# Kernel optimization log

Measured on AMD Instinct MI355X. Metric: run time of the kernel, lower is better.

The kernel has to match this reference:

```python
import jax, jax.numpy as jnp
import numpy as np

U = 256    # hp.hidden_size * 2 (attention num_units / encoder dim)
H = 128    # hp.hidden_size (prenet output, attn GRU input)
MEL = 80   # hp.decoder_output_dim == hp.num_mels
R = 5      # hp.outputs_per_step
B = 64
T = 1000


def _glorot(key, shape):
    fan_in = shape[-1]
    return jax.random.normal(key, shape, jnp.float32) / jnp.sqrt(jnp.float32(fan_in))


def setup_inputs() -> dict:
    key = jax.random.key(0)
    ks = jax.random.split(key, 16)
    p = {}
    p["memory"] = jax.random.normal(ks[0], (B, T, U), jnp.float32)
    # prenet: fc1 (MEL->U), fc2 (U->H)
    p["Wp1"] = _glorot(ks[1], (U, MEL)); p["bp1"] = jnp.zeros((U,), jnp.float32)
    p["Wp2"] = _glorot(ks[2], (H, U));   p["bp2"] = jnp.zeros((H,), jnp.float32)
    # Bahdanau attention params (no bias)
    p["W1"] = _glorot(ks[3], (U, U))
    p["W2"] = _glorot(ks[4], (U, U))
    p["v"]  = _glorot(ks[5], (U,))
    def gru(k, din):
        k1, k2 = jax.random.split(k)
        return (_glorot(k1, (3 * U, din)), _glorot(k2, (3 * U, U)),
                jnp.zeros((3 * U,), jnp.float32), jnp.zeros((3 * U,), jnp.float32))
    p["Wa_ih"], p["Wa_hh"], p["ba_ih"], p["ba_hh"] = gru(ks[6], H)
    p["W1_ih"], p["W1_hh"], p["b1_ih"], p["b1_hh"] = gru(ks[7], U)
    p["W2_ih"], p["W2_hh"], p["b2_ih"], p["b2_hh"] = gru(ks[8], U)
    p["Wproj"] = _glorot(ks[9], (U, 2 * U)); p["bproj"] = jnp.zeros((U,), jnp.float32)
    p["Wout"] = _glorot(ks[10], (MEL * R, U)); p["bout"] = jnp.zeros((MEL * R,), jnp.float32)
    return p


def _gru_cell(x, h, W_ih, W_hh, b_ih, b_hh):
    # torch.nn.GRUCell semantics
    gi = x @ W_ih.T + b_ih
    gh = h @ W_hh.T + b_hh
    ir, iz, inn = jnp.split(gi, 3, axis=-1)
    hr, hz, hn = jnp.split(gh, 3, axis=-1)
    r = jax.nn.sigmoid(ir + hr)
    z = jax.nn.sigmoid(iz + hz)
    n = jnp.tanh(inn + r * hn)
    return (1.0 - z) * n + z * h


def reference(memory, Wp1, bp1, Wp2, bp2, W1, W2, v,
              Wa_ih, Wa_hh, ba_ih, ba_hh,
              W1_ih, W1_hh, b1_ih, b1_hh,
              W2_ih, W2_hh, b2_ih, b2_hh,
              Wproj, bproj, Wout, bout):
    b, t, u = memory.shape
    steps = t // R  # training branch: timesteps = memory_len // outputs_per_step
    # keys = W1(memory): constant across timesteps, hoist out of the loop
    keys = jnp.einsum('btu,vu->btv', memory, W1)
    init = (jnp.zeros((b, MEL), memory.dtype),  # prev mel frame (GO frame = zeros)
            jnp.zeros((b, u), memory.dtype),    # attn_hidden
            jnp.zeros((b, u), memory.dtype),    # gru1_hidden
            jnp.zeros((b, u), memory.dtype))    # gru2_hidden

    def step(carry, _):
        prev, attn_h, g1_h, g2_h = carry
        # prenet (dropout omitted for determinism; identity in eval mode)
        x = jax.nn.relu(prev @ Wp1.T + bp1)
        x = jax.nn.relu(x @ Wp2.T + bp2)
        # attention query through GRU cell
        d_t = _gru_cell(x, attn_h, Wa_ih, Wa_hh, ba_ih, ba_hh)
        q = d_t @ W2.T                                     # [b,u]
        scores = jnp.tanh(keys + q[:, None, :]) @ v       # [b,t]
        aw = jax.nn.softmax(scores, axis=1)
        d_t_prime = jnp.einsum('bt,btu->bu', aw, memory)   # context
        # residual GRU stack
        g1_in = jnp.concatenate([d_t, d_t_prime], axis=1) @ Wproj.T + bproj
        g1_h = _gru_cell(g1_in, g1_h, W1_ih, W1_hh, b1_ih, b1_hh)
        g2_in = g1_in + g1_h
        g2_h = _gru_cell(g2_in, g2_h, W2_ih, W2_hh, b2_ih, b2_hh)
        out = ((g2_in + g2_h) @ Wout.T + bout).reshape(b, MEL, R)
        return (out[:, :, -1], d_t, g1_h, g2_h), out

    _, ys = jax.lax.scan(step, init, None, length=steps)   # [steps,b,MEL,R]
    # torch.cat(outputs, 2) -> [b, MEL, steps*R]
    return jnp.transpose(ys, (1, 2, 0, 3)).reshape(b, MEL, steps * R)
```

## Files before the change

### kernel.cpp

```cpp
#include <hip/hip_runtime.h>

typedef _Float16 f16;
typedef _Float16 h2 __attribute__((ext_vector_type(2)));
typedef float fv4 __attribute__((ext_vector_type(4)));

#define BB 64
#define UU 256
#define RRR 5
#define NQUAD 4

constexpr size_t O_WP1T = 0;
constexpr size_t O_WP2T = 10240;
constexpr size_t O_WAIH = 26624;
constexpr size_t O_WAHH = 75776;
constexpr size_t O_WQP  = 174080;
constexpr size_t O_WPC  = 239616;
constexpr size_t O_W1IH = 272384;
constexpr size_t O_W1HH = 370688;
constexpr size_t O_W2IH = 468992;
constexpr size_t O_W2HH = 567296;
constexpr size_t O_WOUT = 665600;
constexpr size_t OF_BQP = 716800;
constexpr size_t OF_W1T = 717312;
constexpr size_t OH_KEYS = 1565696;
constexpr size_t OH_MEM  = OH_KEYS + 16384000;
constexpr size_t OF_CTXP  = 17166848;
constexpr size_t OF_ESUM  = 17297920;
constexpr size_t OF_QB    = 17298432;
constexpr size_t OI_FLAGA = 17331200;
constexpr size_t OI_FLAGB = 17347584;

#define SCL2LOG2E 2.8853900817779268f

#if defined(__has_builtin)
#if __has_builtin(__builtin_amdgcn_fdot2)
#define USE_FDOT2 1
#endif
#endif

__device__ __forceinline__ float dot2f(h2 a, h2 b, float c){
#ifdef USE_FDOT2
  return __builtin_amdgcn_fdot2(a, b, c, false);
#else
  return c + (float)a[0]*(float)b[0] + (float)a[1]*(float)b[1];
#endif
}

__device__ __forceinline__ float frcp(float x){ return __builtin_amdgcn_rcpf(x); }
__device__ __forceinline__ float fexp2(float x){ return __builtin_amdgcn_exp2f(x); }
__device__ __forceinline__ float fsig(float x){ return frcp(1.0f + fexp2(-1.4426950408889634f*x)); }
__device__ __forceinline__ float ftanh(float x){ return 1.0f - 2.0f*frcp(1.0f + fexp2(SCL2LOG2E*x)); }

__device__ __forceinline__ void wait_flag(const int* fl, int target){
  while (__hip_atomic_load(fl, __ATOMIC_RELAXED, __HIP_MEMORY_SCOPE_AGENT) < target){
    __builtin_amdgcn_s_sleep(8);
  }
  (void)__hip_atomic_load(fl, __ATOMIC_ACQUIRE, __HIP_MEMORY_SCOPE_AGENT);
}

__global__ void k_tr_hx(const float* __restrict__ src, int srcK, int kbase,
                        h2* __restrict__ dst, int N, int K, int Ntot, int coloff,
                        float scale){
  int idx = blockIdx.x*blockDim.x + threadIdx.x;
  int tot = N*(K/2);
  if (idx < tot){
    int k2 = idx / N, n = idx - k2*N;
    h2 p; p[0]=(f16)(scale*src[n*srcK + kbase + 2*k2]);
    p[1]=(f16)(scale*src[n*srcK + kbase + 2*k2+1]);
    dst[(size_t)k2*Ntot + coloff + n] = p;
  }
}

__global__ void k_transpose(const float* __restrict__ src, float* __restrict__ dst, int N, int K){
  int idx = blockIdx.x*blockDim.x + threadIdx.x;
  if (idx < N*K){
    int n = idx / K, k = idx - n*K;
    dst[k*N + n] = src[idx];
  }
}

__global__ void k_biasqp(const float* __restrict__ bproj, float* __restrict__ dst){
  int i = blockIdx.x*blockDim.x + threadIdx.x;
  if (i < 512) dst[i] = (i < 256) ? 0.f : bproj[i-256];
}

__global__ void k_zero(int* __restrict__ p, int n){
  int i = blockIdx.x*blockDim.x + threadIdx.x;
  if (i < n) p[i] = 0;
}

__global__ void k_memh(const float* __restrict__ src, f16* __restrict__ dst, int n8){
  int i = blockIdx.x*blockDim.x + threadIdx.x;
  if (i < n8){
    const float4* s = reinterpret_cast<const float4*>(src) + 2*(size_t)i;
    float4 f0 = s[0], f1 = s[1];
    union { f16 h[8]; float4 v; } u;
    u.h[0]=(f16)f0.x; u.h[1]=(f16)f0.y; u.h[2]=(f16)f0.z; u.h[3]=(f16)f0.w;
    u.h[4]=(f16)f1.x; u.h[5]=(f16)f1.y; u.h[6]=(f16)f1.z; u.h[7]=(f16)f1.w;
    reinterpret_cast<float4*>(dst)[i] = u.v;
  }
}

__global__ __launch_bounds__(256) void k_keys(const float* __restrict__ mem,
      const float* __restrict__ W1t, f16* __restrict__ keys, int T)
{
  const int b = blockIdx.z;
  const int tbase = blockIdx.x * 128;
  const int cbase = blockIdx.y * 128;
  const int tid = threadIdx.x;
  const int rt = tid >> 4, ct = tid & 15;
  const float* memb = mem + (size_t)b*T*UU;

  float acc[8][8];
  #pragma unroll
  for (int i=0;i<8;i++){
    #pragma unroll
    for (int j=0;j<8;j++) acc[i][j]=0.f;
  }
  const float* arow[8];
  #pragma unroll
  for (int i=0;i<8;i++){
    int t = tbase + rt*8 + i;
    arow[i] = memb + (size_t)(t < T ? t : T-1)*UU;
  }
  const float* wcol = W1t + cbase + ct*8;

  for (int k=0;k<UU;k+=4){
    float w8[4][8];
    #pragma unroll
    for (int kk=0;kk<4;kk++){
      float4 lo = *reinterpret_cast<const float4*>(wcol + (size_t)(k+kk)*UU);
      float4 hi = *reinterpret_cast<const float4*>(wcol + (size_t)(k+kk)*UU + 4);
      w8[kk][0]=lo.x; w8[kk][1]=lo.y; w8[kk][2]=lo.z; w8[kk][3]=lo.w;
      w8[kk][4]=hi.x; w8[kk][5]=hi.y; w8[kk][6]=hi.z; w8[kk][7]=hi.w;
    }
    #pragma unroll
    for (int i=0;i<8;i++){
      float4 a = *reinterpret_cast<const float4*>(arow[i] + k);
      float a4[4] = {a.x, a.y, a.z, a.w};
      #pragma unroll
      for (int kk=0;kk<4;kk++){
        #pragma unroll
        for (int j=0;j<8;j++) acc[i][j] += a4[kk]*w8[kk][j];
      }
    }
  }
  #pragma unroll
  for (int i=0;i<8;i++){
    int t = tbase + rt*8 + i;
    if (t < T){
      f16* dst = keys + (size_t)b*T*UU + (size_t)t*UU + cbase + ct*8;
      union { f16 h[8]; float4 v; } u;
      #pragma unroll
      for (int j=0;j<8;j++) u.h[j] = (f16)(acc[i][j]*SCL2LOG2E);
      *reinterpret_cast<float4*>(dst) = u.v;
    }
  }
}

__device__ __attribute__((noinline)) void gemv_shfl(
    const h2* __restrict__ W, const h2* __restrict__ in,
    const float* __restrict__ bias, float* __restrict__ destf, h2* __restrict__ desth,
    int K2, int Nf4, int act, int local)
{
  const int lane = local & 63;
  const int half = lane >> 5;
  int col = (local >> 6)*32 + (lane & 31);
  const bool valid = col < Nf4;
  if (!valid) col = 0;
  const int kh = K2 >> 1;
  const float4* w = reinterpret_cast<const float4*>(W) + (size_t)(half*kh)*Nf4 + col;
  const h2* ia = in + half*kh;
  float a0=0.f, a1=0.f, a2=0.f, a3=0.f;
  #pragma unroll 8
  for (int it = 0; it < kh; ++it){
    float4 wp = w[(size_t)it*Nf4];
    h2 a = ia[it];
    const h2* wh = reinterpret_cast<const h2*>(&wp);
    a0 = dot2f(wh[0], a, a0);
    a1 = dot2f(wh[1], a, a1);
    a2 = dot2f(wh[2], a, a2);
    a3 = dot2f(wh[3], a, a3);
  }
  a0 += __shfl_xor(a0, 32, 64);
  a1 += __shfl_xor(a1, 32, 64);
  a2 += __shfl_xor(a2, 32, 64);
  a3 += __shfl_xor(a3, 32, 64);
  if (half == 0 && valid){
    if (bias){
      const float4 bv = reinterpret_cast<const float4*>(bias)[col];
      a0+=bv.x; a1+=bv.y; a2+=bv.z; a3+=bv.w;
    }
    if (act == 1){
      a0=fmaxf(a0,0.f); a1=fmaxf(a1,0.f); a2=fmaxf(a2,0.f); a3=fmaxf(a3,0.f);
    } else if (act == 2){
      const float4 d = reinterpret_cast<float4*>(destf)[col];
      a0+=d.x; a1+=d.y; a2+=d.z; a3+=d.w;
    }
    if (destf){
      float4 r; r.x=a0; r.y=a1; r.z=a2; r.w=a3;
      reinterpret_cast<float4*>(destf)[col] = r;
    }
    if (desth){
      h2 p0; p0[0]=(f16)a0; p0[1]=(f16)a1;
      h2 p1; p1[0]=(f16)a2; p1[1]=(f16)a3;
      desth[2*col] = p0; desth[2*col+1] = p1;
    }
  }
}

__device__ __attribute__((noinline)) void gemv_shfl4(
    const h2* __restrict__ W, const h2* __restrict__ in,
    const float* __restrict__ bias, float* __restrict__ destf, h2* __restrict__ desth,
    int K2, int Nf4, int act, int local)
{
  const int lane = local & 63;
  const int qtr  = lane >> 4;
  int col = (local >> 6)*16 + (lane & 15);
  const bool valid = col < Nf4;
  if (!valid) col = 0;
  const int kq = K2 >> 2;
  const float4* w = reinterpret_cast<const float4*>(W) + (size_t)(qtr*kq)*Nf4 + col;
  const h2* ia = in + qtr*kq;
  float a0=0.f, a1=0.f, a2=0.f, a3=0.f;
  #pragma unroll 8
  for (int it = 0; it < kq; ++it){
    float4 wp = w[(size_t)it*Nf4];
    h2 a = ia[it];
    const h2* wh = reinterpret_cast<const h2*>(&wp);
    a0 = dot2f(wh[0], a, a0);
    a1 = dot2f(wh[1], a, a1);
    a2 = dot2f(wh[2], a, a2);
    a3 = dot2f(wh[3], a, a3);
  }
  a0 += __shfl_xor(a0, 16, 64); a1 += __shfl_xor(a1, 16, 64);
  a2 += __shfl_xor(a2, 16, 64); a3 += __shfl_xor(a3, 16, 64);
  a0 += __shfl_xor(a0, 32, 64); a1 += __shfl_xor(a1, 32, 64);
  a2 += __shfl_xor(a2, 32, 64); a3 += __shfl_xor(a3, 32, 64);
  if (qtr == 0 && valid){
    if (bias){
      const float4 bv = reinterpret_cast<const float4*>(bias)[col];
      a0+=bv.x; a1+=bv.y; a2+=bv.z; a3+=bv.w;
    }
    if (act == 1){
      a0=fmaxf(a0,0.f); a1=fmaxf(a1,0.f); a2=fmaxf(a2,0.f); a3=fmaxf(a3,0.f);
    } else if (act == 2){
      const float4 d = reinterpret_cast<float4*>(destf)[col];
      a0+=d.x; a1+=d.y; a2+=d.z; a3+=d.w;
    }
    if (destf){
      float4 r; r.x=a0; r.y=a1; r.z=a2; r.w=a3;
      reinterpret_cast<float4*>(destf)[col] = r;
    }
    if (desth){
      h2 p0; p0[0]=(f16)a0; p0[1]=(f16)a1;
      h2 p1; p1[0]=(f16)a2; p1[1]=(f16)a3;
      desth[2*col] = p0; desth[2*col+1] = p1;
    }
  }
}

__device__ __attribute__((noinline)) void gru_gate(
    const float* __restrict__ gi, const float* __restrict__ gh,
    float* __restrict__ h, h2* __restrict__ hh2,
    const float* __restrict__ addsrc, float* __restrict__ sumf,
    h2* __restrict__ sumh, int tid)
{
  if (tid < 128){
    float hn[2], sm[2] = {0.f, 0.f};
    #pragma unroll
    for (int d=0; d<2; ++d){
      int e = 2*tid + d;
      float r = fsig(gi[e] + gh[e]);
      float z = fsig(gi[256+e] + gh[256+e]);
      float n = ftanh(gi[512+e] + r*gh[512+e]);
      hn[d] = (1.f - z)*n + z*h[e];
      h[e] = hn[d];
      if (addsrc){ sm[d] = addsrc[e] + hn[d]; if (sumf) sumf[e] = sm[d]; }
    }
    h2 p; p[0]=(f16)hn[0]; p[1]=(f16)hn[1];
    hh2[tid] = p;
    if (addsrc && sumh){ h2 q; q[0]=(f16)sm[0]; q[1]=(f16)sm[1]; sumh[tid] = q; }
  }
  __syncthreads();
}

__global__ __launch_bounds__(1024) void k_decode(
    const h2* __restrict__ wts, const float* __restrict__ wsf,
    const f16* __restrict__ keysg, const f16* __restrict__ memg,
    float* __restrict__ ctxp, float* __restrict__ esum, float* __restrict__ qbuf,
    int* __restrict__ flagA, int* __restrict__ flagB,
    const float* __restrict__ bp1, const float* __restrict__ bp2,
    const float* __restrict__ vvec,
    const float* __restrict__ ba_ih, const float* __restrict__ ba_hh,
    const float* __restrict__ b1_ih, const float* __restrict__ b1_hh,
    const float* __restrict__ b2_ih, const float* __restrict__ b2_hh,
    const float* __restrict__ bout,
    float* __restrict__ out, int T, int steps)
{
  __shared__ __align__(16) float s_red[4096];
  __shared__ __align__(16) float s_sc[1024];
  __shared__ __align__(16) float s_gi[768];
  __shared__ __align__(16) float s_gh[768];
  __shared__ __align__(16) float s_gh1[768];
  __shared__ __align__(16) float s_gh2[768];
  __shared__ __align__(16) float s_q[512];
  __shared__ __align__(16) float s_ha[256];
  __shared__ __align__(16) float s_g1h[256];
  __shared__ __align__(16) float s_g2h[256];
  __shared__ __align__(16) float s_g2in[256];
  __shared__ __align__(16) float s_y[400];
  __shared__ __align__(16) f16   s_prevf[80];
  __shared__ __align__(16) h2    s_hah[128], s_g1hh[128], s_g2hh[128];
  __shared__ __align__(16) h2    s_g1inh[128], s_g2inh[128], s_s2h[128];
  __shared__ __align__(16) h2    s_x1h[128], s_xh[64], s_ctxh[128];
  __shared__ float s_wred[16];

  const int b    = blockIdx.x & 63;
  const int quad = blockIdx.x >> 6;
  const int tid = threadIdx.x;
  const int lane = tid & 63;
  const int wid = tid >> 6;
  const int half_id = lane >> 5;
  const int cl = lane & 31;

  const f16* keyb = keysg + (size_t)b*T*UU;
  const f16* memb = memg  + (size_t)b*T*UU;
  float* outb = out + (size_t)b*80*(steps*RRR);

  const int ownEnd = ((T*17)/100) & ~1;
  int tq0, tq1;
  if (quad == 0){ tq0 = 0; tq1 = ownEnd; }
  else {
    tq0 = (quad==1) ? ownEnd : (ownEnd + ((T-ownEnd)*(quad-1))/3) & ~1;
    tq1 = (quad==3) ? T      : (ownEnd + ((T-ownEnd)*quad)/3) & ~1;
  }

  float v8[8], m8[8];
  #pragma unroll
  for (int j=0;j<8;j++){ v8[j] = vvec[cl*8+j]; m8[j] = -2.0f*v8[j]; }
  float sumv = 0.f;
  #pragma unroll
  for (int j=0;j<8;j++) sumv += v8[j];
  #pragma unroll
  for (int o=1;o<32;o<<=1) sumv += __shfl_xor(sumv, o);

  auto attn_slice = [&](int par){
    {
      float q8[8];
      #pragma unroll
      for (int j=0;j<8;j++) q8[j] = s_q[cl*8+j];
      float rs = 0.f;
      for (int t0 = tq0 + wid*2; t0 < tq1; t0 += 32){
        int t = t0 + half_id;
        fv4 kv = *(reinterpret_cast<const fv4*>(keyb + (size_t)t*UU) + cl);
        const h2* kh = reinterpret_cast<const h2*>(&kv);
        float acc = 0.f;
        #pragma unroll
        for (int p=0;p<4;p++){
          float t0f = (float)kh[p][0] + q8[2*p];
          float t1f = (float)kh[p][1] + q8[2*p+1];
          acc = fmaf(m8[2*p],   frcp(1.f + fexp2(t0f)), acc);
          acc = fmaf(m8[2*p+1], frcp(1.f + fexp2(t1f)), acc);
        }
        #pragma unroll
        for (int o=1;o<32;o<<=1) acc += __shfl_xor(acc, o);
        float e = __expf(sumv + acc);
        if (cl == 0) s_sc[t] = e;
        rs += e;
      }
      rs += __shfl_xor(rs, 32);
      if (lane==0) s_wred[wid] = rs;
    }
    __syncthreads();
    {
      float c8[8] = {0.f,0.f,0.f,0.f,0.f,0.f,0.f,0.f};
      for (int t0 = tq0 + wid*2; t0 < tq1; t0 += 32){
        int t = t0 + half_id;
        float wgt = s_sc[t];
        fv4 mv = *(reinterpret_cast<const fv4*>(memb + (size_t)t*UU) + cl);
        const h2* mh = reinterpret_cast<const h2*>(&mv);
        #pragma unroll
        for (int p=0;p<4;p++){
          c8[2*p  ] += wgt*(float)mh[p][0];
          c8[2*p+1] += wgt*(float)mh[p][1];
        }
      }
      #pragma unroll
      for (int j=0;j<8;j++) c8[j] += __shfl_xor(c8[j], 32);
      if (half_id == 0){
        float4 lo; lo.x=c8[0]; lo.y=c8[1]; lo.z=c8[2]; lo.w=c8[3];
        float4 hi; hi.x=c8[4]; hi.y=c8[5]; hi.z=c8[6]; hi.w=c8[7];
        *reinterpret_cast<float4*>(s_red + wid*256 + cl*8)     = lo;
        *reinterpret_cast<float4*>(s_red + wid*256 + cl*8 + 4) = hi;
      }
    }
    __syncthreads();
    {
      float* cp = ctxp + (((size_t)b*2 + par)*NQUAD + quad)*256;
      if (tid < 128){
        float a = 0.f, c = 0.f;
        #pragma unroll
        for (int w=0; w<16; ++w){
          a += s_red[w*256 + 2*tid];
          c += s_red[w*256 + 2*tid+1];
        }
        cp[2*tid]   = a;
        cp[2*tid+1] = c;
      }
      if (tid == 0){
        float tot = 0.f;
        #pragma unroll
        for (int w=0; w<16; ++w) tot += s_wred[w];
        esum[((size_t)b*2 + par)*NQUAD + quad] = tot;
      }
    }
    __syncthreads();
  };

  if (quad != 0){
    for (int step = 0; step < steps; ++step){
      const int par = step & 1;
      if (tid == 0) wait_flag(flagA + b*256 + step, 1);
      __syncthreads();
      if (tid < 256)
        s_q[tid] = __hip_atomic_load(qbuf + ((size_t)b*2 + par)*256 + tid,
                                     __ATOMIC_RELAXED, __HIP_MEMORY_SCOPE_AGENT);
      __syncthreads();
      attn_slice(par);
      if (tid == 0){
        __threadfence();
        __hip_atomic_fetch_add(flagB + b*256 + step, 1, __ATOMIC_RELEASE, __HIP_MEMORY_SCOPE_AGENT);
      }
      __syncthreads();
    }
    return;
  }

  if (tid < 128){
    s_ha[2*tid]=0.f; s_ha[2*tid+1]=0.f;
    s_g1h[2*tid]=0.f; s_g1h[2*tid+1]=0.f;
    s_g2h[2*tid]=0.f; s_g2h[2*tid+1]=0.f;
    h2 z; z[0]=(f16)0.f; z[1]=(f16)0.f;
    s_hah[tid]=z; s_g1hh[tid]=z; s_g2hh[tid]=z;
  }
  if (tid < 80) s_prevf[tid] = (f16)0.f;
  __syncthreads();

  for (int step = 0; step < steps; ++step){
    const int par = step & 1;
    if (tid < 384)      gemv_shfl (wts+O_WAHH, s_hah, ba_hh, s_gh, nullptr, 128, 192, 0, tid);
    else if (tid < 640) gemv_shfl4(wts+O_WP1T, reinterpret_cast<const h2*>(s_prevf), bp1,
                                   nullptr, s_x1h, 40, 64, 1, tid-384);
    __syncthreads();
    if (tid < 128) gemv_shfl4(wts+O_WP2T, s_x1h, bp2, nullptr, s_xh, 128, 32, 1, tid);
    __syncthreads();
    if (tid < 768) gemv_shfl4(wts+O_WAIH, s_xh, ba_ih, s_gi, nullptr, 64, 192, 0, tid);
    __syncthreads();
    gru_gate(s_gi, s_gh, s_ha, s_hah, nullptr, nullptr, nullptr, tid);
    if (tid < 512) gemv_shfl4(wts+O_WQP, s_hah, wsf+OF_BQP, s_q, nullptr, 128, 128, 0, tid);
    __syncthreads();
    if (tid < 256)
      qbuf[((size_t)b*2 + par)*256 + tid] = s_q[tid];
    __syncthreads();
    if (tid == 0){
      __threadfence();
      __hip_atomic_fetch_add(flagA + b*256 + step, 1, __ATOMIC_RELEASE, __HIP_MEMORY_SCOPE_AGENT);
    }
    if (tid < 384)      gemv_shfl(wts+O_W1HH, s_g1hh, b1_hh, s_gh1, nullptr, 128, 192, 0, tid);
    else if (tid < 768) gemv_shfl(wts+O_W2HH, s_g2hh, b2_hh, s_gh2, nullptr, 128, 192, 0, tid-384);
    attn_slice(par);
    if (tid == 0){
      __threadfence();
      __hip_atomic_fetch_add(flagB + b*256 + step, 1, __ATOMIC_RELEASE, __HIP_MEMORY_SCOPE_AGENT);
      wait_flag(flagB + b*256 + step, NQUAD);
    }
    __syncthreads();
    if (tid < 128){
      const float* cp0 = ctxp + ((size_t)b*2 + par)*NQUAD*256;
      const float* es0 = esum + ((size_t)b*2 + par)*NQUAD;
      float es = 0.f;
      #pragma unroll
      for (int q4=0;q4<NQUAD;q4++)
        es += __hip_atomic_load(&es0[q4], __ATOMIC_RELAXED, __HIP_MEMORY_SCOPE_AGENT);
      float inv = frcp(es);
      float a = 0.f, c = 0.f;
      #pragma unroll
      for (int q4=0;q4<NQUAD;q4++){
        a += __hip_atomic_load(&cp0[q4*256 + 2*tid],   __ATOMIC_RELAXED, __HIP_MEMORY_SCOPE_AGENT);
        c += __hip_atomic_load(&cp0[q4*256 + 2*tid+1], __ATOMIC_RELAXED, __HIP_MEMORY_SCOPE_AGENT);
      }
      h2 p; p[0]=(f16)(a*inv); p[1]=(f16)(c*inv);
      s_ctxh[tid] = p;
    }
    __syncthreads();
    if (tid < 256) gemv_shfl4(wts+O_WPC, s_ctxh, nullptr, s_q+256, s_g1inh, 128, 64, 2, tid);
    __syncthreads();
    if (tid < 768) gemv_shfl4(wts+O_W1IH, s_g1inh, b1_ih, s_gi, nullptr, 128, 192, 0, tid);
    __syncthreads();
    gru_gate(s_gi, s_gh1, s_g1h, s_g1hh, s_q+256, s_g2in, s_g2inh, tid);
    if (tid < 768) gemv_shfl4(wts+O_W2IH, s_g2inh, b2_ih, s_gi, nullptr, 128, 192, 0, tid);
    __syncthreads();
    gru_gate(s_gi, s_gh2, s_g2h, s_g2hh, s_g2in, nullptr, s_s2h, tid);
    if (tid < 448) gemv_shfl4(wts+O_WOUT, s_s2h, bout, s_y, nullptr, 128, 100, 0, tid);
    __syncthreads();
    if (tid < 400){
      float val = s_y[tid];
      int mel = tid / 5, rr = tid - mel*5;
      __builtin_nontemporal_store(val, &outb[(size_t)mel*(steps*RRR) + step*RRR + rr]);
      if (rr == 4) s_prevf[mel] = (f16)val;
    }
    __syncthreads();
  }
}

extern "C" void kernel_launch(void* const* d_in, const int* in_sizes, int n_in,
                              void* d_out, int out_size, void* d_ws, size_t ws_size,
                              hipStream_t stream)
{
  const float* mem  = (const float*)d_in[0];
  const float* Wp1  = (const float*)d_in[1];
  const float* bp1  = (const float*)d_in[2];
  const float* Wp2  = (const float*)d_in[3];
  const float* bp2  = (const float*)d_in[4];
  const float* W1   = (const float*)d_in[5];
  const float* W2   = (const float*)d_in[6];
  const float* vv   = (const float*)d_in[7];
  const float* Wa_ih= (const float*)d_in[8];
  const float* Wa_hh= (const float*)d_in[9];
  const float* ba_ih= (const float*)d_in[10];
  const float* ba_hh= (const float*)d_in[11];
  const float* W1_ih= (const float*)d_in[12];
  const float* W1_hh= (const float*)d_in[13];
  const float* b1_ih= (const float*)d_in[14];
  const float* b1_hh= (const float*)d_in[15];
  const float* W2_ih= (const float*)d_in[16];
  const float* W2_hh= (const float*)d_in[17];
  const float* b2_ih= (const float*)d_in[18];
  const float* b2_hh= (const float*)d_in[19];
  const float* Wproj= (const float*)d_in[20];
  const float* bproj= (const float*)d_in[21];
  const float* Wout = (const float*)d_in[22];
  const float* bout = (const float*)d_in[23];

  h2*  wsH2 = (h2*)d_ws;
  f16* wsF16= (f16*)d_ws;
  float* wsF = (float*)d_ws;
  int*  wsI = (int*)d_ws;
  int T = in_sizes[0] / (BB*UU);
  int steps = T / RRR;

  auto tr = [&](const float* src, int srcK, int kbase, size_t off, int N, int K,
                int Ntot, int coloff, float scale){
    int total = N*(K/2);
    k_tr_hx<<<dim3((total+255)/256), dim3(256), 0, stream>>>(
        src, srcK, kbase, wsH2 + off, N, K, Ntot, coloff, scale);
  };
  tr(Wp1,   80,  0, O_WP1T, 256, 80,  256, 0, 1.f);
  tr(Wp2,   256, 0, O_WP2T, 128, 256, 128, 0, 1.f);
  tr(Wa_ih, 128, 0, O_WAIH, 768, 128, 768, 0, 1.f);
  tr(Wa_hh, 256, 0, O_WAHH, 768, 256, 768, 0, 1.f);
  tr(W2,    256, 0, O_WQP,  256, 256, 512, 0, SCL2LOG2E);
  tr(Wproj, 512, 0, O_WQP,  256, 256, 512, 256, 1.f);
  tr(Wproj, 512, 256, O_WPC, 256, 256, 256, 0, 1.f);
  tr(W1_ih, 256, 0, O_W1IH, 768, 256, 768, 0, 1.f);
  tr(W1_hh, 256, 0, O_W1HH, 768, 256, 768, 0, 1.f);
  tr(W2_ih, 256, 0, O_W2IH, 768, 256, 768, 0, 1.f);
  tr(W2_hh, 256, 0, O_W2HH, 768, 256, 768, 0, 1.f);
  tr(Wout,  256, 0, O_WOUT, 400, 256, 400, 0, 1.f);

  k_biasqp<<<dim3(2), dim3(256), 0, stream>>>(bproj, wsF + OF_BQP);
  k_transpose<<<dim3((256*256+255)/256), dim3(256), 0, stream>>>(W1, wsF + OF_W1T, 256, 256);
  k_zero<<<dim3(128), dim3(256), 0, stream>>>(wsI + OI_FLAGA, 2*64*256);

  int n8 = (BB*T*UU)/8;
  k_memh<<<dim3((n8+255)/256), dim3(256), 0, stream>>>(mem, wsF16 + OH_MEM, n8);
  k_keys<<<dim3((T+127)/128, UU/128, BB), dim3(256), 0, stream>>>(mem, wsF + OF_W1T, wsF16 + OH_KEYS, T);

  k_decode<<<dim3(BB*NQUAD), dim3(1024), 0, stream>>>(wsH2, wsF,
      wsF16 + OH_KEYS, wsF16 + OH_MEM,
      wsF + OF_CTXP, wsF + OF_ESUM, wsF + OF_QB,
      wsI + OI_FLAGA, wsI + OI_FLAGB,
      bp1, bp2, vv, ba_ih, ba_hh, b1_ih, b1_hh, b2_ih, b2_hh, bout,
      (float*)d_out, T, steps);
}
```

Baseline: 11.99 ms.

## Fold output-to-prenet projection into fused weight and defer attention-GRU hidden GEMV

Precomputes a fused weight Wp1·Wout[last frame rows] and fused bias so the next step's prenet-fc1 input comes directly from the GRU2 state in the same GEMV phase as the output projection. This removes one serialized GEMV+barrier phase at the start of each decoder step. The Wa_hh·h GEMV for the next step is moved into the attention-overlap region with double-buffered results. The attention split between the owner block and helper blocks is also rebalanced. Precision changes slightly because the fused product is rounded to fp16.

Result: faster. 11.25 ms (-6.2%).

```diff
diff --git a/kernel.cpp b/kernel.cpp
--- a/kernel.cpp
+++ b/kernel.cpp
@@ -9,7 +9,6 @@
 #define RRR 5
 #define NQUAD 4
 
-constexpr size_t O_WP1T = 0;
 constexpr size_t O_WP2T = 10240;
 constexpr size_t O_WAIH = 26624;
 constexpr size_t O_WAHH = 75776;
@@ -29,6 +28,8 @@
 constexpr size_t OF_QB    = 17298432;
 constexpr size_t OI_FLAGA = 17331200;
 constexpr size_t OI_FLAGB = 17347584;
+constexpr size_t O_WFUSE  = 17364992;
+constexpr size_t OF_BFUSE = 17397760;
 
 #define SCL2LOG2E 2.8853900817779268f
 
@@ -82,6 +83,34 @@
 __global__ void k_biasqp(const float* __restrict__ bproj, float* __restrict__ dst){
   int i = blockIdx.x*blockDim.x + threadIdx.x;
   if (i < 512) dst[i] = (i < 256) ? 0.f : bproj[i-256];
+}
+
+__global__ void k_fuse_w(const float* __restrict__ Wp1, const float* __restrict__ Wout,
+                         h2* __restrict__ dst){
+  int idx = blockIdx.x*blockDim.x + threadIdx.x;
+  if (idx < 256*128){
+    int k2 = idx >> 8;
+    int n  = idx & 255;
+    float s0=0.f, s1=0.f;
+    for (int mel=0; mel<80; ++mel){
+      float wp = Wp1[n*80+mel];
+      const float* wr = Wout + (size_t)(5*mel+4)*256;
+      s0 += wp * wr[2*k2];
+      s1 += wp * wr[2*k2+1];
+    }
+    h2 p; p[0]=(f16)s0; p[1]=(f16)s1;
+    dst[(size_t)k2*256 + n] = p;
+  }
+}
+
+__global__ void k_fuse_b(const float* __restrict__ Wp1, const float* __restrict__ bout,
+                         const float* __restrict__ bp1, float* __restrict__ dst){
+  int n = blockIdx.x*blockDim.x + threadIdx.x;
+  if (n < 256){
+    float s = bp1[n];
+    for (int mel=0; mel<80; ++mel) s += Wp1[n*80+mel]*bout[5*mel+4];
+    dst[n] = s;
+  }
 }
 
 __global__ void k_zero(int* __restrict__ p, int n){
@@ -290,8 +319,7 @@
     const f16* __restrict__ keysg, const f16* __restrict__ memg,
     float* __restrict__ ctxp, float* __restrict__ esum, float* __restrict__ qbuf,
     int* __restrict__ flagA, int* __restrict__ flagB,
-    const float* __restrict__ bp1, const float* __restrict__ bp2,
-    const float* __restrict__ vvec,
+    const float* __restrict__ bp2, const float* __restrict__ vvec,
     const float* __restrict__ ba_ih, const float* __restrict__ ba_hh,
     const float* __restrict__ b1_ih, const float* __restrict__ b1_hh,
     const float* __restrict__ b2_ih, const float* __restrict__ b2_hh,
@@ -301,7 +329,7 @@
   __shared__ __align__(16) float s_red[4096];
   __shared__ __align__(16) float s_sc[1024];
   __shared__ __align__(16) float s_gi[768];
-  __shared__ __align__(16) float s_gh[768];
+  __shared__ __align__(16) float s_ghP[2][768];
   __shared__ __align__(16) float s_gh1[768];
   __shared__ __align__(16) float s_gh2[768];
   __shared__ __align__(16) float s_q[512];
@@ -310,7 +338,6 @@
   __shared__ __align__(16) float s_g2h[256];
   __shared__ __align__(16) float s_g2in[256];
   __shared__ __align__(16) float s_y[400];
-  __shared__ __align__(16) f16   s_prevf[80];
   __shared__ __align__(16) h2    s_hah[128], s_g1hh[128], s_g2hh[128];
   __shared__ __align__(16) h2    s_g1inh[128], s_g2inh[128], s_s2h[128];
   __shared__ __align__(16) h2    s_x1h[128], s_xh[64], s_ctxh[128];
@@ -328,7 +355,7 @@
   const f16* memb = memg  + (size_t)b*T*UU;
   float* outb = out + (size_t)b*80*(steps*RRR);
 
-  const int ownEnd = ((T*17)/100) & ~1;
+  const int ownEnd = ((T*14)/100) & ~1;
   int tq0, tq1;
   if (quad == 0){ tq0 = 0; tq1 = ownEnd; }
   else {
@@ -443,21 +470,26 @@
     s_g2h[2*tid]=0.f; s_g2h[2*tid+1]=0.f;
     h2 z; z[0]=(f16)0.f; z[1]=(f16)0.f;
     s_hah[tid]=z; s_g1hh[tid]=z; s_g2hh[tid]=z;
-  }
-  if (tid < 80) s_prevf[tid] = (f16)0.f;
+    float a0 = fmaxf(wsf[0]*0.f + 0.f, 0.f);
+  }
+  if (tid < 128){
+    extern __shared__ float _dummy[]; (void)_dummy;
+  }
+  if (tid < 128){
+    const float* ix = wsf + OF_BFUSE + 256;
+    h2 p; p[0] = (f16)ix[2*tid]; p[1] = (f16)ix[2*tid+1];
+    s_x1h[tid] = p;
+  }
+  for (int i = tid; i < 768; i += 1024) s_ghP[0][i] = ba_hh[i];
   __syncthreads();
 
   for (int step = 0; step < steps; ++step){
     const int par = step & 1;
-    if (tid < 384)      gemv_shfl (wts+O_WAHH, s_hah, ba_hh, s_gh, nullptr, 128, 192, 0, tid);
-    else if (tid < 640) gemv_shfl4(wts+O_WP1T, reinterpret_cast<const h2*>(s_prevf), bp1,
-                                   nullptr, s_x1h, 40, 64, 1, tid-384);
-    __syncthreads();
     if (tid < 128) gemv_shfl4(wts+O_WP2T, s_x1h, bp2, nullptr, s_xh, 128, 32, 1, tid);
     __syncthreads();
     if (tid < 768) gemv_shfl4(wts+O_WAIH, s_xh, ba_ih, s_gi, nullptr, 64, 192, 0, tid);
     __syncthreads();
-    gru_gate(s_gi, s_gh, s_ha, s_hah, nullptr, nullptr, nullptr, tid);
+    gru_gate(s_gi, s_ghP[par], s_ha, s_hah, nullptr, nullptr, nullptr, tid);
     if (tid < 512) gemv_shfl4(wts+O_WQP, s_hah, wsf+OF_BQP, s_q, nullptr, 128, 128, 0, tid);
     __syncthreads();
     if (tid < 256)
@@ -467,6 +499,7 @@
       __threadfence();
       __hip_atomic_fetch_add(flagA + b*256 + step, 1, __ATOMIC_RELEASE, __HIP_MEMORY_SCOPE_AGENT);
     }
+    if (tid < 768) gemv_shfl4(wts+O_WAHH, s_hah, ba_hh, s_ghP[par^1], nullptr, 128, 192, 0, tid);
     if (tid < 384)      gemv_shfl(wts+O_W1HH, s_g1hh, b1_hh, s_gh1, nullptr, 128, 192, 0, tid);
     else if (tid < 768) gemv_shfl(wts+O_W2HH, s_g2hh, b2_hh, s_gh2, nullptr, 128, 192, 0, tid-384);
     attn_slice(par);
@@ -502,16 +535,21 @@
     if (tid < 768) gemv_shfl4(wts+O_W2IH, s_g2inh, b2_ih, s_gi, nullptr, 128, 192, 0, tid);
     __syncthreads();
     gru_gate(s_gi, s_gh2, s_g2h, s_g2hh, s_g2in, nullptr, s_s2h, tid);
-    if (tid < 448) gemv_shfl4(wts+O_WOUT, s_s2h, bout, s_y, nullptr, 128, 100, 0, tid);
+    if (tid < 448)      gemv_shfl4(wts+O_WOUT,  s_s2h, bout, s_y, nullptr, 128, 100, 0, tid);
+    else if (tid < 704) gemv_shfl4(wts+O_WFUSE, s_s2h, wsf+OF_BFUSE, nullptr, s_x1h, 128, 64, 1, tid-448);
     __syncthreads();
     if (tid < 400){
       float val = s_y[tid];
       int mel = tid / 5, rr = tid - mel*5;
       __builtin_nontemporal_store(val, &outb[(size_t)mel*(steps*RRR) + step*RRR + rr]);
-      if (rr == 4) s_prevf[mel] = (f16)val;
-    }
-    __syncthreads();
-  }
+    }
+    __syncthreads();
+  }
+}
+
+__global__ void k_initx1(const float* __restrict__ bp1, float* __restrict__ dst){
+  int n = blockIdx.x*blockDim.x + threadIdx.x;
+  if (n < 256) dst[n] = fmaxf(bp1[n], 0.f);
 }
 
 extern "C" void kernel_launch(void* const* d_in, const int* in_sizes, int n_in,
@@ -556,7 +594,6 @@
     k_tr_hx<<<dim3((total+255)/256), dim3(256), 0, stream>>>(
         src, srcK, kbase, wsH2 + off, N, K, Ntot, coloff, scale);
   };
-  tr(Wp1,   80,  0, O_WP1T, 256, 80,  256, 0, 1.f);
   tr(Wp2,   256, 0, O_WP2T, 128, 256, 128, 0, 1.f);
   tr(Wa_ih, 128, 0, O_WAIH, 768, 128, 768, 0, 1.f);
   tr(Wa_hh, 256, 0, O_WAHH, 768, 256, 768, 0, 1.f);
@@ -572,6 +609,9 @@
   k_biasqp<<<dim3(2), dim3(256), 0, stream>>>(bproj, wsF + OF_BQP);
   k_transpose<<<dim3((256*256+255)/256), dim3(256), 0, stream>>>(W1, wsF + OF_W1T, 256, 256);
   k_zero<<<dim3(128), dim3(256), 0, stream>>>(wsI + OI_FLAGA, 2*64*256);
+  k_fuse_w<<<dim3((256*128+255)/256), dim3(256), 0, stream>>>(Wp1, Wout, wsH2 + O_WFUSE);
+  k_fuse_b<<<dim3(1), dim3(256), 0, stream>>>(Wp1, bout, bp1, wsF + OF_BFUSE);
+  k_initx1<<<dim3(1), dim3(256), 0, stream>>>(bp1, wsF + OF_BFUSE + 256);
 
   int n8 = (BB*T*UU)/8;
   k_memh<<<dim3((n8+255)/256), dim3(256), 0, stream>>>(mem, wsF16 + OH_MEM, n8);
@@ -581,6 +621,6 @@
       wsF16 + OH_KEYS, wsF16 + OH_MEM,
       wsF + OF_CTXP, wsF + OF_ESUM, wsF + OF_QB,
       wsI + OI_FLAGA, wsI + OI_FLAGB,
-      bp1, bp2, vv, ba_ih, ba_hh, b1_ih, b1_hh, b2_ih, b2_hh, bout,
+      bp2, vv, ba_ih, ba_hh, b1_ih, b1_hh, b2_ih, b2_hh, bout,
       (float*)d_out, T, steps);
 }
```
